# Optimization experiments

Hardware: AMD Instinct MI355X
Metric: run time of the kernel (lower is better)

## Reference

```python
import jax, jax.numpy as jnp
import numpy as np

Z, P, CIN, COUT, E, HID = 4, 512, 32, 32, 65536, 128

def setup_inputs() -> dict:
    key = jax.random.key(0)
    ks = jax.random.split(key, 8)
    return {
        "features": jax.random.normal(ks[0], (Z, P, CIN), dtype=jnp.float32),
        "edge_vec": jax.random.normal(ks[1], (E, 3), dtype=jnp.float32),
        "W1": jax.random.normal(ks[2], (4, HID), dtype=jnp.float32) * 0.5,
        "b1": jax.random.normal(ks[3], (HID,), dtype=jnp.float32) * 0.1,
        "W2": jax.random.normal(ks[4], (HID, COUT * CIN), dtype=jnp.float32) * (1.0 / np.sqrt(HID)),
        "edge_batch": jax.random.randint(ks[5], (E,), 0, Z),
        "edge_a": jax.random.randint(ks[6], (E,), 0, P),
        "edge_b": jax.random.randint(ks[7], (E,), 0, P),
        "n_norm": 1,
    }

def reference(features, edge_vec, W1, b1, W2, edge_batch, edge_a, edge_b, n_norm):
    Zb, Pn, Cin = features.shape
    # zero near-degenerate radii (matches radius[norm < 1e-10] = 0)
    r = jnp.linalg.norm(edge_vec, axis=-1, keepdims=True)  # [E,1]
    vec = jnp.where(r < 1e-10, jnp.zeros_like(edge_vec), edge_vec)
    rn = jnp.where(r < 1e-10, jnp.zeros_like(r), r)
    # per-edge kernel: MLP(vec, |vec|) -> [E, c_out, c_in]
    x = jnp.concatenate([vec, rn], axis=-1)               # [E,4]
    h = jax.nn.relu(x @ W1 + b1)                          # [E,HID]
    Cout = W2.shape[1] // Cin
    k = (h @ W2).reshape(-1, Cout, Cin)                   # [E,co,ci]
    # gather neighbor features, per-edge matvec, scatter-add to centers
    f_b = features[edge_batch, edge_b]                    # [E,ci]
    msg = jnp.einsum('eij,ej->ei', k, f_b)                # [E,co]
    seg = edge_batch * Pn + edge_a
    out = jax.ops.segment_sum(msg, seg, num_segments=Zb * Pn)
    out = out.reshape(Zb, Pn, Cout)
    return out / jnp.sqrt(jnp.asarray(n_norm, dtype=features.dtype))
```

## Files before the change

### kernel.cpp

```cpp
#include <hip/hip_runtime.h>

#define ZBATCH 4
#define PN     512
#define CINC   32
#define COUTC  32
#define EN     65536
#define HIDN   128
#define NNODE  (ZBATCH*PN)
#define CAP    128
#define WFW    2048

using hvec2 = decltype(__builtin_amdgcn_cvt_pkrtz(0.f, 0.f));
typedef __attribute__((ext_vector_type(8))) _Float16 f16x8;
typedef __attribute__((ext_vector_type(4))) float f32x4;

static __device__ __forceinline__ unsigned packh2(float a, float b) {
  hvec2 h = __builtin_amdgcn_cvt_pkrtz(a, b);
  unsigned u;
  __builtin_memcpy(&u, &h, 4);
  return u;
}

__global__ __launch_bounds__(256) void k1_bin_wf(
    const float* __restrict__ F, const float* __restrict__ W2,
    unsigned* __restrict__ Wf, const int* __restrict__ eb,
    const int* __restrict__ ea, const int* __restrict__ ebn,
    int* __restrict__ cnt_src, int* __restrict__ cnt_dst,
    int* __restrict__ order_src, int* __restrict__ order_dst) {
  const int t = threadIdx.x;
  const int b = blockIdx.x;
  if (b < 256) {
    const int e = b * 256 + t;
    const int zb = eb[e];
    const int ns = zb * PN + ebn[e];
    const int nd = zb * PN + ea[e];
    const int p = atomicAdd(&cnt_src[ns], 1);
    if (p < CAP) order_src[ns * CAP + p] = e;
    const int q = atomicAdd(&cnt_dst[nd], 1);
    if (q < CAP) order_dst[nd * CAP + q] = e;
    return;
  }
  const int bb = b - 256;
  const int jt = bb & 7, ntile = bb >> 3;
  const int hp = t & 63;
  const int co = jt * 4 + (t >> 6);
  const int ks = hp >> 4, g = (hp >> 2) & 3, j = hp & 3;
  const int nt = co >> 4, col = co & 15;
  const int flat = (ks * 2 + nt) * 256 + g * 64 + col * 4 + j;
  const float4* rA = (const float4*)(W2 + (size_t)(2 * hp) * (COUTC * CINC)
                                     + co * CINC);
  const float4* rB = (const float4*)(W2 + (size_t)(2 * hp + 1) * (COUTC * CINC)
                                     + co * CINC);
  float4 wa[8], wb[8];
#pragma unroll
  for (int q = 0; q < 8; ++q) { wa[q] = rA[q]; wb[q] = rB[q]; }
  const int n0 = ntile * 32;
  for (int n = 0; n < 32; ++n) {
    const float4* fr = (const float4*)(F + (size_t)(n0 + n) * CINC);
    float a0 = 0.f, a1 = 0.f, a2 = 0.f, a3 = 0.f;
    float c0 = 0.f, c1 = 0.f, c2 = 0.f, c3 = 0.f;
#pragma unroll
    for (int q = 0; q < 8; ++q) {
      const float4 f = fr[q];
      a0 = fmaf(f.x, wa[q].x, a0); a1 = fmaf(f.y, wa[q].y, a1);
      a2 = fmaf(f.z, wa[q].z, a2); a3 = fmaf(f.w, wa[q].w, a3);
      c0 = fmaf(f.x, wb[q].x, c0); c1 = fmaf(f.y, wb[q].y, c1);
      c2 = fmaf(f.z, wb[q].z, c2); c3 = fmaf(f.w, wb[q].w, c3);
    }
    Wf[(size_t)(n0 + n) * WFW + flat] =
        packh2((a0 + a1) + (a2 + a3), (c0 + c1) + (c2 + c3));
  }
}

__global__ __launch_bounds__(256) void k2_msg(
    const float* __restrict__ evec, const float* __restrict__ W1,
    const float* __restrict__ b1, const unsigned* __restrict__ Wf,
    const int* __restrict__ cnt_src, const int* __restrict__ order_src,
    const int* __restrict__ nn, float* __restrict__ msg) {
  const int t = threadIdx.x;
  const int lane = t & 63, w = t >> 6;
  const int n = blockIdx.x * 2 + (w >> 1);
  const int q = w & 1;
  const int col = lane & 15, g = lane >> 4;

  __shared__ __align__(16) unsigned Hb[4][1024];

  const int c0 = cnt_src[n];
  const int count = c0 < CAP ? c0 : CAP;
  if (count <= q * 16) return;

  f16x8 bf[8];
  {
    const unsigned* wfb = Wf + (size_t)n * WFW + g * 64 + col * 4;
#pragma unroll
    for (int q8 = 0; q8 < 8; ++q8) {
      const uint4 braw = *(const uint4*)(wfb + q8 * 256);
      __builtin_memcpy(&bf[q8], &braw, 16);
    }
  }
  const int h0 = lane << 1;
  const float2 u0 = *(const float2*)(W1 + 0 * HIDN + h0);
  const float2 u1 = *(const float2*)(W1 + 1 * HIDN + h0);
  const float2 u2 = *(const float2*)(W1 + 2 * HIDN + h0);
  const float2 u3 = *(const float2*)(W1 + 3 * HIDN + h0);
  const float2 b2 = *(const float2*)(b1 + h0);
  const float scale = rsqrtf((float)nn[0]);

  for (int base = q * 16; base < count; base += 32) {
    int ordv = 0;
    if (lane < 16) {
      const int idx = base + lane;
      const int ii = idx < count ? idx : count - 1;
      ordv = order_src[(size_t)n * CAP + ii];
    }
#pragma unroll
    for (int i = 0; i < 16; ++i) {
      unsigned word = 0;
      if (base + i < count) {
        const int e = __builtin_amdgcn_readlane(ordv, i);
        const float x0 = evec[3 * e], x1 = evec[3 * e + 1], x2 = evec[3 * e + 2];
        const float r2 = sqrtf(x0 * x0 + x1 * x1 + x2 * x2);
        const bool bad = (r2 < 1e-10f);
        const float y0 = bad ? 0.f : x0, y1 = bad ? 0.f : x1;
        const float y2 = bad ? 0.f : x2, y3 = bad ? 0.f : r2;
        const float a0 = fmaf(y3, u3.x, fmaf(y2, u2.x,
                         fmaf(y1, u1.x, fmaf(y0, u0.x, b2.x))));
        const float a1 = fmaf(y3, u3.y, fmaf(y2, u2.y,
                         fmaf(y1, u1.y, fmaf(y0, u0.y, b2.y))));
        word = packh2(fmaxf(a0, 0.f), fmaxf(a1, 0.f));
      }
      Hb[w][(unsigned)(i * 64 + lane) ^ ((unsigned)(i & 7) << 2)] = word;
    }
    __builtin_amdgcn_wave_barrier();
    f32x4 acc0 = {0.f, 0.f, 0.f, 0.f};
    f32x4 acc1 = {0.f, 0.f, 0.f, 0.f};
    const unsigned axor = (unsigned)((col & 7) << 2);
#pragma unroll
    for (int ks = 0; ks < 4; ++ks) {
      const unsigned aidx = ((unsigned)(col * 64 + ks * 16 + g * 4)) ^ axor;
      const uint4 araw = *(const uint4*)&Hb[w][aidx];
      f16x8 af;
      __builtin_memcpy(&af, &araw, 16);
      acc0 = __builtin_amdgcn_mfma_f32_16x16x32_f16(af, bf[ks * 2 + 0], acc0, 0, 0, 0);
      acc1 = __builtin_amdgcn_mfma_f32_16x16x32_f16(af, bf[ks * 2 + 1], acc1, 0, 0, 0);
    }
    __builtin_amdgcn_wave_barrier();
#pragma unroll
    for (int r = 0; r < 4; ++r) {
      const int row = g * 4 + r;
      const int gi = base + row;
      if (gi < count) {
        const int e = __shfl(ordv, row);
        msg[(size_t)e * COUTC + col]      = acc0[r] * scale;
        msg[(size_t)e * COUTC + 16 + col] = acc1[r] * scale;
      }
    }
    __builtin_amdgcn_wave_barrier();
  }
}

__global__ __launch_bounds__(256) void k3_reduce(
    const float* __restrict__ msg, const int* __restrict__ cnt_dst,
    const int* __restrict__ order_dst, float* __restrict__ out) {
  const int t = threadIdx.x;
  const int lane = t & 63, w = t >> 6;
  const int co = lane & 31, hh = lane >> 5;
  const int n = blockIdx.x * 4 + w;
  __shared__ int idxs[4][CAP];
  const int c0 = cnt_dst[n];
  const int count = c0 < CAP ? c0 : CAP;
  for (int i = lane; i < count; i += 64)
    idxs[w][i] = order_dst[(size_t)n * CAP + i];
  __builtin_amdgcn_wave_barrier();
  float a0 = 0.f, a1 = 0.f, a2 = 0.f, a3 = 0.f;
  for (int gq = hh * 4; gq < count; gq += 8) {
    const int i1 = gq + 1, i2 = gq + 2, i3 = gq + 3;
    a0 += msg[(size_t)idxs[w][gq] * COUTC + co];
    if (i1 < count) a1 += msg[(size_t)idxs[w][i1] * COUTC + co];
    if (i2 < count) a2 += msg[(size_t)idxs[w][i2] * COUTC + co];
    if (i3 < count) a3 += msg[(size_t)idxs[w][i3] * COUTC + co];
  }
  float acc = (a0 + a1) + (a2 + a3);
  acc += __shfl_xor(acc, 32);
  if (hh == 0) out[(size_t)n * COUTC + co] = acc;
}

extern "C" void kernel_launch(void* const* d_in, const int* in_sizes, int n_in,
                              void* d_out, int out_size, void* d_ws, size_t ws_size,
                              hipStream_t stream) {
  const float* features   = (const float*)d_in[0];
  const float* edge_vec   = (const float*)d_in[1];
  const float* W1         = (const float*)d_in[2];
  const float* b1         = (const float*)d_in[3];
  const float* W2         = (const float*)d_in[4];
  const int*   edge_batch = (const int*)d_in[5];
  const int*   edge_a     = (const int*)d_in[6];
  const int*   edge_b     = (const int*)d_in[7];
  const int*   n_norm     = (const int*)d_in[8];
  float* out = (float*)d_out;

  char* ws = (char*)d_ws;
  unsigned* Wf = (unsigned*)ws;
  float* msg = (float*)(ws + (size_t)NNODE * WFW * 4);
  int* ints = (int*)(ws + (size_t)NNODE * WFW * 4 + (size_t)EN * COUTC * 4);
  int* cnt_src   = ints;
  int* cnt_dst   = ints + NNODE;
  int* order_src = ints + 2 * NNODE;
  int* order_dst = order_src + NNODE * CAP;
  const size_t need = (size_t)NNODE * WFW * 4 + (size_t)EN * COUTC * 4
                    + (size_t)(2 * NNODE + 2 * NNODE * CAP) * 4;
  if (ws_size < need) return;

  (void)hipMemsetAsync(cnt_src, 0, 2 * NNODE * 4, stream);
  k1_bin_wf<<<256 + 512, 256, 0, stream>>>(features, W2, Wf, edge_batch,
                                           edge_a, edge_b, cnt_src, cnt_dst,
                                           order_src, order_dst);
  k2_msg<<<NNODE / 2, 256, 0, stream>>>(edge_vec, W1, b1, Wf, cnt_src,
                                        order_src, n_norm, msg);
  k3_reduce<<<NNODE / 4, 256, 0, stream>>>(msg, cnt_dst, order_dst, out);
}
```

Baseline: 135.1 us.

## Compute first MLP layer with MFMA instead of scalar per-edge FMAs

The hidden layer (edge features times W1 plus bias, then ReLU) was computed per edge in a 16-step scalar loop using readlane broadcasts. Now each of 16 lanes loads one edge's vector, packs it as fp16 into an MFMA A operand zero-padded to K=32, and eight 16x16x32 MFMAs produce the 16x128 hidden tile. Results are written to LDS as fp16 halves with a new swizzle. This trades scalar VALU work and serialized loads for matrix ops and 2-byte LDS stores, and lowers input precision of the edge vector and W1 to fp16.

```diff
diff --git a/kernel.cpp b/kernel.cpp
--- a/kernel.cpp
+++ b/kernel.cpp
@@ -83,7 +83,7 @@
   const int q = w & 1;
   const int col = lane & 15, g = lane >> 4;
 
-  __shared__ __align__(16) unsigned Hb[4][1024];
+  __shared__ __align__(16) unsigned short Hb[4][16 * 128];
 
   const int c0 = cnt_src[n];
   const int count = c0 < CAP ? c0 : CAP;
@@ -98,51 +98,75 @@
       __builtin_memcpy(&bf[q8], &braw, 16);
     }
   }
-  const int h0 = lane << 1;
-  const float2 u0 = *(const float2*)(W1 + 0 * HIDN + h0);
-  const float2 u1 = *(const float2*)(W1 + 1 * HIDN + h0);
-  const float2 u2 = *(const float2*)(W1 + 2 * HIDN + h0);
-  const float2 u3 = *(const float2*)(W1 + 3 * HIDN + h0);
-  const float2 b2 = *(const float2*)(b1 + h0);
+  f16x8 w1b[8];
+  float b1v[8];
+#pragma unroll
+  for (int nt = 0; nt < 8; ++nt) {
+    const int h = nt * 16 + col;
+    b1v[nt] = b1[h];
+    unsigned four[4] = {0u, 0u, 0u, 0u};
+    if (g == 0) {
+      four[0] = packh2(W1[h],            W1[HIDN + h]);
+      four[1] = packh2(W1[2 * HIDN + h], W1[3 * HIDN + h]);
+    }
+    __builtin_memcpy(&w1b[nt], four, 16);
+  }
   const float scale = rsqrtf((float)nn[0]);
+  unsigned short* hbase = &Hb[w][0];
 
   for (int base = q * 16; base < count; base += 32) {
     int ordv = 0;
+    float y0 = 0.f, y1 = 0.f, y2 = 0.f, y3 = 0.f;
     if (lane < 16) {
       const int idx = base + lane;
       const int ii = idx < count ? idx : count - 1;
       ordv = order_src[(size_t)n * CAP + ii];
-    }
-#pragma unroll
-    for (int i = 0; i < 16; ++i) {
-      unsigned word = 0;
-      if (base + i < count) {
-        const int e = __builtin_amdgcn_readlane(ordv, i);
-        const float x0 = evec[3 * e], x1 = evec[3 * e + 1], x2 = evec[3 * e + 2];
-        const float r2 = sqrtf(x0 * x0 + x1 * x1 + x2 * x2);
-        const bool bad = (r2 < 1e-10f);
-        const float y0 = bad ? 0.f : x0, y1 = bad ? 0.f : x1;
-        const float y2 = bad ? 0.f : x2, y3 = bad ? 0.f : r2;
-        const float a0 = fmaf(y3, u3.x, fmaf(y2, u2.x,
-                         fmaf(y1, u1.x, fmaf(y0, u0.x, b2.x))));
-        const float a1 = fmaf(y3, u3.y, fmaf(y2, u2.y,
-                         fmaf(y1, u1.y, fmaf(y0, u0.y, b2.y))));
-        word = packh2(fmaxf(a0, 0.f), fmaxf(a1, 0.f));
+      const float x0 = evec[3 * ordv], x1 = evec[3 * ordv + 1],
+                  x2 = evec[3 * ordv + 2];
+      const float r2 = sqrtf(x0 * x0 + x1 * x1 + x2 * x2);
+      const bool bad = (r2 < 1e-10f);
+      y0 = bad ? 0.f : x0; y1 = bad ? 0.f : x1;
+      y2 = bad ? 0.f : x2; y3 = bad ? 0.f : r2;
+    }
+    f16x8 af;
+    {
+      unsigned four[4] = {0u, 0u, 0u, 0u};
+      if (lane < 16) {
+        four[0] = packh2(y0, y1);
+        four[1] = packh2(y2, y3);
       }
-      Hb[w][(unsigned)(i * 64 + lane) ^ ((unsigned)(i & 7) << 2)] = word;
+      __builtin_memcpy(&af, four, 16);
+    }
+#pragma unroll
+    for (int nt = 0; nt < 8; ++nt) {
+      f32x4 ah = {b1v[nt], b1v[nt], b1v[nt], b1v[nt]};
+      ah = __builtin_amdgcn_mfma_f32_16x16x32_f16(af, w1b[nt], ah, 0, 0, 0);
+#pragma unroll
+      for (int r = 0; r < 4; ++r) {
+        const float hv = fmaxf(ah[r], 0.f);
+        const int e = g * 4 + r;
+        const unsigned baddr =
+            ((unsigned)(e * 256 + (nt * 16 + col) * 2)) ^
+            ((unsigned)(e & 7) << 4);
+        __fp16 h16 = (__fp16)hv;
+        unsigned short bits;
+        __builtin_memcpy(&bits, &h16, 2);
+        *(unsigned short*)((char*)hbase + baddr) = bits;
+      }
     }
     __builtin_amdgcn_wave_barrier();
     f32x4 acc0 = {0.f, 0.f, 0.f, 0.f};
     f32x4 acc1 = {0.f, 0.f, 0.f, 0.f};
-    const unsigned axor = (unsigned)((col & 7) << 2);
 #pragma unroll
     for (int ks = 0; ks < 4; ++ks) {
-      const unsigned aidx = ((unsigned)(col * 64 + ks * 16 + g * 4)) ^ axor;
-      const uint4 araw = *(const uint4*)&Hb[w][aidx];
-      f16x8 af;
-      __builtin_memcpy(&af, &araw, 16);
-      acc0 = __builtin_amdgcn_mfma_f32_16x16x32_f16(af, bf[ks * 2 + 0], acc0, 0, 0, 0);
-      acc1 = __builtin_amdgcn_mfma_f32_16x16x32_f16(af, bf[ks * 2 + 1], acc1, 0, 0, 0);
+      const unsigned raddr =
+          ((unsigned)(col * 256 + ks * 64 + g * 16)) ^
+          ((unsigned)(col & 7) << 4);
+      const uint4 araw = *(const uint4*)((char*)hbase + raddr);
+      f16x8 a2;
+      __builtin_memcpy(&a2, &araw, 16);
+      acc0 = __builtin_amdgcn_mfma_f32_16x16x32_f16(a2, bf[ks * 2 + 0], acc0, 0, 0, 0);
+      acc1 = __builtin_amdgcn_mfma_f32_16x16x32_f16(a2, bf[ks * 2 + 1], acc1, 0, 0, 0);
     }
     __builtin_amdgcn_wave_barrier();
 #pragma unroll
```

Result: faster. 130.9 us (-3.1%).
